# Performance work log

Measured on AMD Instinct MI355X. Metric: run time of the kernel, lower is better.

The kernel has to match this reference:

```python
import jax, jax.numpy as jnp
import numpy as np
import math

B, N, Q, K = 1, 64, 512, 512
C_Q = C_K = C_V = 256
C_HIDDEN = 32
NO_HEADS = 8
HID = C_HIDDEN * NO_HEADS  # 256


def setup_inputs() -> dict:
    key = jax.random.key(0)
    ks = jax.random.split(key, 12)
    inp = {
        "q_x": jax.random.normal(ks[0], (B, N, Q, C_Q), jnp.float32),
        "k_x": jax.random.normal(ks[1], (B, N, K, C_K), jnp.float32),
        "v_x": jax.random.normal(ks[2], (B, N, K, C_V), jnp.float32),
        "bias_mask": jax.random.normal(ks[3], (B, N, 1, 1, K), jnp.float32),
        "bias_pair": jax.random.normal(ks[4], (B, 1, NO_HEADS, Q, K), jnp.float32),
        # projection weights stored [in, out] (torch Linear is [out, in])
        "wq": jax.random.normal(ks[5], (C_Q, HID), jnp.float32) / math.sqrt(C_Q),
        "wk": jax.random.normal(ks[6], (C_K, HID), jnp.float32) / math.sqrt(C_K),
        "wv": jax.random.normal(ks[7], (C_V, HID), jnp.float32) / math.sqrt(C_V),
        # gating: init weights=0, bias=1 in the module; use small random for a non-trivial test
        "wg": jax.random.normal(ks[8], (C_Q, HID), jnp.float32) * 0.02,
        "bg": jnp.ones((HID,), jnp.float32),
        # output: init 'final' (zeros); use small random for a non-trivial test
        "wo": jax.random.normal(ks[9], (HID, C_Q), jnp.float32) * 0.02,
        "bo": jnp.zeros((C_Q,), jnp.float32),
    }
    return inp


def reference(q_x, k_x, v_x, bias_mask, bias_pair, wq, wk, wv, wg, bg, wo, bo):
    h, c = NO_HEADS, C_HIDDEN
    # projections -> [B, N, Q/K, H, C_h]
    q = (q_x @ wq).reshape(*q_x.shape[:-1], h, c) / math.sqrt(c)
    k = (k_x @ wk).reshape(*k_x.shape[:-1], h, c)
    v = (v_x @ wv).reshape(*v_x.shape[:-1], h, c)
    # logits [B, N, H, Q, K] with additive biases
    a = jnp.einsum("bnqhc,bnkhc->bnhqk", q, k) + bias_mask + bias_pair
    a = jax.nn.softmax(a, axis=-1)
    # output [B, N, Q, H, C_h]
    o = jnp.einsum("bnhqk,bnkhc->bnqhc", a, v)
    # gating
    g = jax.nn.sigmoid((q_x @ wg + bg).reshape(*q_x.shape[:-1], h, c))
    o = o * g
    o = o.reshape(*o.shape[:-2], h * c)
    return o @ wo + bo
```

## Files before the change

kernel.cpp:

```cpp
#include <hip/hip_runtime.h>
#include <math.h>

#define NSEQ   64
#define QLEN   512
#define KLEN   512
#define CIN    256
#define HEADS  8
#define CH     32
#define HIDDIM 256
#define M_TOTAL (NSEQ * QLEN)
#define L2E    1.4426950408889634f

typedef _Float16 f16x8 __attribute__((ext_vector_type(8)));
typedef _Float16 f16x4 __attribute__((ext_vector_type(4)));
typedef __fp16   fp16x2 __attribute__((ext_vector_type(2)));
typedef float    f32x4 __attribute__((ext_vector_type(4)));

__device__ __forceinline__ void gload16(const void* g, void* l) {
    __builtin_amdgcn_global_load_lds(
        (const __attribute__((address_space(1))) void*)g,
        (__attribute__((address_space(3))) void*)l, 16, 0, 0);
}

__device__ __forceinline__ float exp2_fast(float x) {
#if __has_builtin(__builtin_amdgcn_exp2f)
    return __builtin_amdgcn_exp2f(x);
#else
    float r; asm("v_exp_f32 %0, %1" : "=v"(r) : "v"(x)); return r;
#endif
}

__global__ __launch_bounds__(256) void wcast_kernel(
    const float* __restrict__ w0, const float* __restrict__ w1,
    const float* __restrict__ w2, const float* __restrict__ w3,
    const float* __restrict__ w4, _Float16* __restrict__ wt)
{
    __shared__ float t[64][65];
    const float* W;
    switch (blockIdx.z) {
        case 0: W = w0; break; case 1: W = w1; break;
        case 2: W = w2; break; case 3: W = w3; break;
        default: W = w4;
    }
    _Float16* WT = wt + (size_t)blockIdx.z * 65536;
    const int i0 = blockIdx.x * 64, o0 = blockIdx.y * 64;
    const int tid = threadIdx.x;
    const int rr = tid >> 4, c4 = tid & 15;
    #pragma unroll
    for (int i = 0; i < 4; ++i) {
        const int row = rr + i * 16;
        *(float4*)&t[row][c4 * 4] = *(const float4*)&W[(size_t)(i0 + row) * 256 + o0 + c4 * 4];
    }
    __syncthreads();
    #pragma unroll
    for (int i = 0; i < 4; ++i) {
        const int row = rr + i * 16;
        f16x4 v;
        #pragma unroll
        for (int j = 0; j < 4; ++j) v[j] = (_Float16)t[c4 * 4 + j][row];
        *(f16x4*)&WT[(size_t)(o0 + row) * 256 + i0 + c4 * 4] = v;
    }
}

__global__ __launch_bounds__(256) void bpfrag_kernel(
    const float* __restrict__ bias_pair, float* __restrict__ frag)
{
    __shared__ float t[64][68];
    const int qb = blockIdx.x, kb = blockIdx.y, h = blockIdx.z;
    const int tid = threadIdx.x;
    #pragma unroll
    for (int i = 0; i < 4; ++i) {
        const int idx = tid + i * 256;
        const int r = idx >> 4, c4 = idx & 15;
        *(float4*)&t[r][c4 * 4] = *(const float4*)
            &bias_pair[((size_t)h * QLEN + qb * 64 + r) * KLEN + kb * 64 + c4 * 4];
    }
    __syncthreads();
    const int lane = tid & 63, w = tid >> 6;
    const int l15 = lane & 15, quad = lane >> 4;
    const int qt = qb * 4 + w;
    #pragma unroll
    for (int kt2 = 0; kt2 < 4; ++kt2) {
        const int kt = kb * 4 + kt2;
        float4 v;
        v.x = (t[w * 16 + l15][kt2 * 16 + quad * 4 + 0] - 4.0f) * L2E;
        v.y = (t[w * 16 + l15][kt2 * 16 + quad * 4 + 1] - 4.0f) * L2E;
        v.z = (t[w * 16 + l15][kt2 * 16 + quad * 4 + 2] - 4.0f) * L2E;
        v.w = (t[w * 16 + l15][kt2 * 16 + quad * 4 + 3] - 4.0f) * L2E;
        *(float4*)&frag[(((size_t)(h * 32 + qt) * 32) + kt) * 256 + lane * 4] = v;
    }
}

__global__ __launch_bounds__(256) void bmscale_kernel(
    const float* __restrict__ bm, float* __restrict__ o)
{
    const int i = blockIdx.x * 256 + threadIdx.x;
    float4 v = *(const float4*)(bm + (size_t)i * 4);
    v.x *= L2E; v.y *= L2E; v.z *= L2E; v.w *= L2E;
    *(float4*)(o + (size_t)i * 4) = v;
}

__global__ __launch_bounds__(256, 3) void proj_gemm_kernel(
    const float* __restrict__ q_x, const float* __restrict__ k_x,
    const float* __restrict__ v_x, const _Float16* __restrict__ wT,
    const float* __restrict__ bg,
    _Float16* __restrict__ oq, _Float16* __restrict__ ok,
    _Float16* __restrict__ ovT, _Float16* __restrict__ og)
{
    __shared__ __attribute__((aligned(16))) _Float16 A_s[2][32 * 256];

    const int combo = blockIdx.x >> 6;
    const int blk   = blockIdx.x & 63;
    const int mode  = combo >> 1;
    const int nhalf = combo & 1;
    const float* A = (mode <= 1) ? q_x : (mode == 2) ? k_x : v_x;
    const _Float16* BT = wT + (size_t)mode * 65536;

    const int tid  = threadIdx.x;
    const int lane = tid & 63, w = tid >> 6;
    const int l15  = lane & 15, quad = lane >> 4;
    const int nw   = nhalf * 128 + w * 32;

    f16x8 bfr[2][8];
    #pragma unroll
    for (int nt = 0; nt < 2; ++nt)
        #pragma unroll
        for (int ks = 0; ks < 8; ++ks)
            bfr[nt][ks] = *(const f16x8*)(BT +
                (size_t)(nw + nt * 16 + l15) * 256 + ks * 32 + quad * 8);

    float bgv[2] = {0.f, 0.f};
    if (mode == 1) { bgv[0] = bg[nw + l15]; bgv[1] = bg[nw + 16 + l15]; }

    const int row_base = blk * 512;

    f32x4 acc[2][2];
    #pragma unroll
    for (int mt = 0; mt < 2; ++mt)
        #pragma unroll
        for (int nt = 0; nt < 2; ++nt) acc[mt][nt] = (f32x4){0.f, 0.f, 0.f, 0.f};

    float4 sreg[8];

    auto gload_panel = [&](int panel) {
        const int row0 = row_base + panel * 32;
        #pragma unroll
        for (int j = 0; j < 4; ++j) {
            const int p = tid + j * 256;
            const int r = p >> 5, c = p & 31;
            const float* ap = A + (size_t)(row0 + r) * 256 + c * 8;
            sreg[j * 2]     = *(const float4*)ap;
            sreg[j * 2 + 1] = *(const float4*)(ap + 4);
        }
    };

    auto swrite_panel = [&](int buf) {
        #pragma unroll
        for (int j = 0; j < 4; ++j) {
            const int p = tid + j * 256;
            const int r = p >> 5, c = p & 31;
            const int cp = c ^ (r & 15);
            f16x8 v;
            v[0] = (_Float16)sreg[j * 2].x;     v[1] = (_Float16)sreg[j * 2].y;
            v[2] = (_Float16)sreg[j * 2].z;     v[3] = (_Float16)sreg[j * 2].w;
            v[4] = (_Float16)sreg[j * 2 + 1].x; v[5] = (_Float16)sreg[j * 2 + 1].y;
            v[6] = (_Float16)sreg[j * 2 + 1].z; v[7] = (_Float16)sreg[j * 2 + 1].w;
            *(f16x8*)&A_s[buf][(r * 32 + cp) * 8] = v;
        }
    };

    gload_panel(0);
    swrite_panel(0);
    __syncthreads();

    for (int i = 0; i < 16; ++i) {
        const int buf = i & 1;
        if (i < 15) gload_panel(i + 1);

        #pragma unroll
        for (int ks = 0; ks < 8; ++ks) {
            f16x8 af[2];
            #pragma unroll
            for (int mt = 0; mt < 2; ++mt) {
                const int r  = mt * 16 + l15;
                const int cp = (ks * 4 + quad) ^ (r & 15);
                af[mt] = *(const f16x8*)&A_s[buf][(r * 32 + cp) * 8];
            }
            #pragma unroll
            for (int mt = 0; mt < 2; ++mt)
                #pragma unroll
                for (int nt = 0; nt < 2; ++nt)
                    acc[mt][nt] = __builtin_amdgcn_mfma_f32_16x16x32_f16(
                        af[mt], bfr[nt][ks], acc[mt][nt], 0, 0, 0);
        }

        const int row0 = row_base + i * 32;
        if (mode == 3) {
            #pragma unroll
            for (int mt = 0; mt < 2; ++mt) {
                #pragma unroll
                for (int nt = 0; nt < 2; ++nt) {
                    const int col  = nw + nt * 16 + l15;
                    const int rowg = row0 + mt * 16 + quad * 4;
                    const int nn = rowg >> 9, kpos = rowg & 511;
                    f16x4 st;
                    #pragma unroll
                    for (int reg = 0; reg < 4; ++reg) st[reg] = (_Float16)acc[mt][nt][reg];
                    *(f16x4*)&ovT[((size_t)(nn * 256 + col)) * 512 + kpos] = st;
                }
            }
        } else {
            _Float16* C = (mode == 0) ? oq : (mode == 1) ? og : ok;
            #pragma unroll
            for (int mt = 0; mt < 2; ++mt) {
                #pragma unroll
                for (int nt = 0; nt < 2; ++nt) {
                    const int col  = nw + nt * 16 + l15;
                    const int rowg = row0 + mt * 16 + quad * 4;
                    #pragma unroll
                    for (int reg = 0; reg < 4; ++reg) {
                        float x = acc[mt][nt][reg];
                        if (mode == 0) x *= 0.2550348614f;
                        if (mode == 1) { x += bgv[nt]; x = 1.0f / (1.0f + __expf(-x)); }
                        C[(size_t)(rowg + reg) * HIDDIM + col] = (_Float16)x;
                    }
                }
            }
        }
        #pragma unroll
        for (int mt = 0; mt < 2; ++mt)
            #pragma unroll
            for (int nt = 0; nt < 2; ++nt) acc[mt][nt] = (f32x4){0.f, 0.f, 0.f, 0.f};

        if (i < 15) swrite_panel(buf ^ 1);
        __syncthreads();
    }
}

__global__ __launch_bounds__(256, 2) void outproj_kernel(
    const _Float16* __restrict__ Ain, const _Float16* __restrict__ BT,
    const float* __restrict__ bias, float* __restrict__ Cout)
{
    __shared__ __attribute__((aligned(16))) _Float16 A_s[2][32 * 256];

    const int blk   = blockIdx.x & 255;
    const int nhalf = blockIdx.x >> 8;
    const int tid  = threadIdx.x;
    const int lane = tid & 63, w = tid >> 6;
    const int l15  = lane & 15, quad = lane >> 4;
    const int nw   = nhalf * 128 + w * 32;

    f16x8 bfr[2][8];
    #pragma unroll
    for (int nt = 0; nt < 2; ++nt)
        #pragma unroll
        for (int ks = 0; ks < 8; ++ks)
            bfr[nt][ks] = *(const f16x8*)(BT +
                (size_t)(nw + nt * 16 + l15) * 256 + ks * 32 + quad * 8);

    const float bv[2] = { bias[nw + l15], bias[nw + 16 + l15] };
    const int row_base = blk * 128;

    f32x4 acc[2][2];
    #pragma unroll
    for (int mt = 0; mt < 2; ++mt)
        #pragma unroll
        for (int nt = 0; nt < 2; ++nt) acc[mt][nt] = (f32x4){0.f, 0.f, 0.f, 0.f};

    auto stage = [&](int panel, int buf) {
        const int row0 = row_base + panel * 32;
        #pragma unroll
        for (int j = 0; j < 4; ++j) {
            const int p = tid + j * 256;
            const int r = p >> 5, c = p & 31;
            const int cl = (c & ~7) | ((c & 7) ^ (r & 7));
            gload16(Ain + (size_t)(row0 + r) * 256 + cl * 8, &A_s[buf][p * 8]);
        }
    };

    stage(0, 0);
    __syncthreads();

    for (int i = 0; i < 4; ++i) {
        if (i < 3) stage(i + 1, (i + 1) & 1);
        const int buf = i & 1;

        #pragma unroll
        for (int ks = 0; ks < 8; ++ks) {
            f16x8 af[2];
            #pragma unroll
            for (int mt = 0; mt < 2; ++mt) {
                const int r = mt * 16 + l15;
                const int c = (ks * 4 + quad) ^ (r & 7);
                af[mt] = *(const f16x8*)&A_s[buf][r * 256 + c * 8];
            }
            #pragma unroll
            for (int mt = 0; mt < 2; ++mt)
                #pragma unroll
                for (int nt = 0; nt < 2; ++nt)
                    acc[mt][nt] = __builtin_amdgcn_mfma_f32_16x16x32_f16(
                        af[mt], bfr[nt][ks], acc[mt][nt], 0, 0, 0);
        }

        const int row0 = row_base + i * 32;
        #pragma unroll
        for (int mt = 0; mt < 2; ++mt) {
            #pragma unroll
            for (int nt = 0; nt < 2; ++nt) {
                const int col  = nw + nt * 16 + l15;
                const int rowg = row0 + mt * 16 + quad * 4;
                #pragma unroll
                for (int reg = 0; reg < 4; ++reg)
                    Cout[(size_t)(rowg + reg) * HIDDIM + col] = acc[mt][nt][reg] + bv[nt];
            }
        }
        #pragma unroll
        for (int mt = 0; mt < 2; ++mt)
            #pragma unroll
            for (int nt = 0; nt < 2; ++nt) acc[mt][nt] = (f32x4){0.f, 0.f, 0.f, 0.f};

        __syncthreads();
    }
}

__global__ __launch_bounds__(256, 4) void attn_kernel(
    const _Float16* __restrict__ qb, const _Float16* __restrict__ kb,
    const _Float16* __restrict__ vT, const _Float16* __restrict__ gb,
    _Float16* __restrict__ ob,
    const float* __restrict__ bm2, const float* __restrict__ bp_frag)
{
    __shared__ _Float16 k_s[128][40];
    __shared__ _Float16 v_s[32][136];

    const int n    = blockIdx.x;
    const int h    = blockIdx.y;
    const int q0   = blockIdx.z * 128;
    const int tid  = threadIdx.x;
    const int lane = tid & 63;
    const int wq   = tid >> 6;
    const int l15  = lane & 15;
    const int quad = lane >> 4;

    f16x8 qf[2];
    #pragma unroll
    for (int qt = 0; qt < 2; ++qt)
        qf[qt] = *(const f16x8*)(qb +
            (size_t)(n * QLEN + q0 + wq * 32 + qt * 16 + l15) * HIDDIM + h * CH + quad * 8);

    const float* bpf = bp_frag +
        ((size_t)(h * 32 + blockIdx.z * 8 + wq * 2) * 32) * 256 + lane * 4;
    const float* bmb = bm2 + n * KLEN + quad * 4;

    f32x4 o_acc[2][2];
    float l_lane[2] = {0.f, 0.f};
    #pragma unroll
    for (int qt = 0; qt < 2; ++qt)
        #pragma unroll
        for (int ct = 0; ct < 2; ++ct) o_acc[qt][ct] = (f32x4){0.f, 0.f, 0.f, 0.f};

    for (int ch = 0; ch < 4; ++ch) {
        __syncthreads();
        #pragma unroll
        for (int i = 0; i < 2; ++i) {
            const int idx = tid + i * 256;
            const int r = idx >> 2, c8 = idx & 3;
            *(uint4*)&k_s[r][c8 * 8] = *(const uint4*)
                (kb + (size_t)(n * KLEN + ch * 128 + r) * HIDDIM + h * CH + c8 * 8);
            const int vr = idx >> 4, vs = idx & 15;
            *(uint4*)&v_s[vr][vs * 8] = *(const uint4*)
                (vT + ((size_t)(n * HEADS + h) * CH + vr) * KLEN + ch * 128 + vs * 8);
        }
        __syncthreads();

        #pragma unroll
        for (int kt = 0; kt < 8; ++kt) {
            const int kti = ch * 8 + kt;
            const f16x8 kf = *(const f16x8*)&k_s[kt * 16 + l15][quad * 8];
            const float4 bm  = *(const float4*)(bmb + ch * 128 + kt * 16);
            const float4 bp0 = *(const float4*)(bpf + (size_t)kti * 256);
            const float4 bp1 = *(const float4*)(bpf + (size_t)(32 + kti) * 256);
            f32x4 c0, c1;
            c0[0] = bm.x + bp0.x; c0[1] = bm.y + bp0.y;
            c0[2] = bm.z + bp0.z; c0[3] = bm.w + bp0.w;
            c1[0] = bm.x + bp1.x; c1[1] = bm.y + bp1.y;
            c1[2] = bm.z + bp1.z; c1[3] = bm.w + bp1.w;
            __builtin_amdgcn_s_setprio(1);
            const f32x4 s0 = __builtin_amdgcn_mfma_f32_16x16x32_f16(kf, qf[0], c0, 0, 0, 0);
            const f32x4 s1 = __builtin_amdgcn_mfma_f32_16x16x32_f16(kf, qf[1], c1, 0, 0, 0);
            __builtin_amdgcn_s_setprio(0);
            const f16x4 bv0 = *(const f16x4*)&v_s[l15][kt * 16 + quad * 4];
            const f16x4 bv1 = *(const f16x4*)&v_s[16 + l15][kt * 16 + quad * 4];
            #pragma unroll
            for (int qt = 0; qt < 2; ++qt) {
                const f32x4 s = qt ? s1 : s0;
                const float p0 = exp2_fast(s[0]);
                const float p1 = exp2_fast(s[1]);
                const float p2 = exp2_fast(s[2]);
                const float p3 = exp2_fast(s[3]);
                l_lane[qt] += (p0 + p1) + (p2 + p3);
                union { f16x4 v; fp16x2 h[2]; } u;
                u.h[0] = __builtin_amdgcn_cvt_pkrtz(p0, p1);
                u.h[1] = __builtin_amdgcn_cvt_pkrtz(p2, p3);
                __builtin_amdgcn_s_setprio(1);
                o_acc[qt][0] = __builtin_amdgcn_mfma_f32_16x16x16f16(u.v, bv0, o_acc[qt][0], 0, 0, 0);
                o_acc[qt][1] = __builtin_amdgcn_mfma_f32_16x16x16f16(u.v, bv1, o_acc[qt][1], 0, 0, 0);
                __builtin_amdgcn_s_setprio(0);
            }
        }
    }

    float invl[2][4];
    #pragma unroll
    for (int qt = 0; qt < 2; ++qt) {
        float lf = l_lane[qt];
        lf += __shfl_xor(lf, 16);
        lf += __shfl_xor(lf, 32);
        #pragma unroll
        for (int reg = 0; reg < 4; ++reg)
            invl[qt][reg] = 1.0f / __shfl(lf, quad * 4 + reg);
    }

    #pragma unroll
    for (int qt = 0; qt < 2; ++qt) {
        #pragma unroll
        for (int ct = 0; ct < 2; ++ct) {
            #pragma unroll
            for (int reg = 0; reg < 4; ++reg) {
                const int row = q0 + wq * 32 + qt * 16 + quad * 4 + reg;
                const size_t idx = (size_t)(n * QLEN + row) * HIDDIM + h * CH + ct * 16 + l15;
                const float g = (float)gb[idx];
                ob[idx] = (_Float16)(o_acc[qt][ct][reg] * invl[qt][reg] * g);
            }
        }
    }
}

extern "C" void kernel_launch(void* const* d_in, const int* in_sizes, int n_in,
                              void* d_out, int out_size, void* d_ws, size_t ws_size,
                              hipStream_t stream)
{
    const float* q_x       = (const float*)d_in[0];
    const float* k_x       = (const float*)d_in[1];
    const float* v_x       = (const float*)d_in[2];
    const float* bias_mask = (const float*)d_in[3];
    const float* bias_pair = (const float*)d_in[4];
    const float* wq        = (const float*)d_in[5];
    const float* wk        = (const float*)d_in[6];
    const float* wv        = (const float*)d_in[7];
    const float* wg        = (const float*)d_in[8];
    const float* bg        = (const float*)d_in[9];
    const float* wo        = (const float*)d_in[10];
    const float* bo        = (const float*)d_in[11];
    float* out = (float*)d_out;

    const size_t BUF = (size_t)M_TOTAL * HIDDIM;
    _Float16* ws_q  = (_Float16*)d_ws;
    _Float16* ws_k  = ws_q + BUF;
    _Float16* ws_vT = ws_k + BUF;
    _Float16* ws_g  = ws_vT + BUF;
    _Float16* ws_o  = ws_g + BUF;
    _Float16* wT    = ws_o + BUF;
    float*    bpf   = (float*)(wT + 5 * 65536);
    float*    bm2   = bpf + (size_t)8 * 512 * 512;

    wcast_kernel<<<dim3(4, 4, 5), 256, 0, stream>>>(wq, wg, wk, wv, wo, wT);
    bpfrag_kernel<<<dim3(8, 8, 8), 256, 0, stream>>>(bias_pair, bpf);
    bmscale_kernel<<<dim3(32), 256, 0, stream>>>(bias_mask, bm2);

    proj_gemm_kernel<<<dim3(512), 256, 0, stream>>>(
        q_x, k_x, v_x, wT, bg, ws_q, ws_k, ws_vT, ws_g);

    attn_kernel<<<dim3(NSEQ, HEADS, QLEN / 128), 256, 0, stream>>>(
        ws_q, ws_k, ws_vT, ws_g, ws_o, bm2, bpf);

    outproj_kernel<<<dim3(512), 256, 0, stream>>>(
        ws_o, wT + 4 * 65536, bo, out);
}
```

Baseline: 257.6 us.

## Swap MFMA operands for row-contiguous vector stores and double GEMM grid sizes

In the projection and output GEMMs, the MFMA operand order is swapped so each lane holds four consecutive columns of one row. The epilogue can then write f16x4 or float4 vector stores instead of scattered scalar stores; the bias is loaded as float4 to match. The grid of both GEMM kernels is doubled, with half the rows per block, to add parallelism, and the output-projection occupancy hint is raised to 3. The trade-off is that the per-block weight-fragment register load is amortized over fewer rows.

```diff
diff --git a/kernel.cpp b/kernel.cpp
--- a/kernel.cpp
+++ b/kernel.cpp
@@ -109,8 +109,8 @@
 {
     __shared__ __attribute__((aligned(16))) _Float16 A_s[2][32 * 256];
 
-    const int combo = blockIdx.x >> 6;
-    const int blk   = blockIdx.x & 63;
+    const int combo = blockIdx.x >> 7;
+    const int blk   = blockIdx.x & 127;
     const int mode  = combo >> 1;
     const int nhalf = combo & 1;
     const float* A = (mode <= 1) ? q_x : (mode == 2) ? k_x : v_x;
@@ -129,10 +129,13 @@
             bfr[nt][ks] = *(const f16x8*)(BT +
                 (size_t)(nw + nt * 16 + l15) * 256 + ks * 32 + quad * 8);
 
-    float bgv[2] = {0.f, 0.f};
-    if (mode == 1) { bgv[0] = bg[nw + l15]; bgv[1] = bg[nw + 16 + l15]; }
-
-    const int row_base = blk * 512;
+    float4 bg4[2] = {{0.f,0.f,0.f,0.f},{0.f,0.f,0.f,0.f}};
+    if (mode == 1) {
+        bg4[0] = *(const float4*)&bg[nw + quad * 4];
+        bg4[1] = *(const float4*)&bg[nw + 16 + quad * 4];
+    }
+
+    const int row_base = blk * 256;
 
     f32x4 acc[2][2];
     #pragma unroll
@@ -173,9 +176,9 @@
     swrite_panel(0);
     __syncthreads();
 
-    for (int i = 0; i < 16; ++i) {
+    for (int i = 0; i < 8; ++i) {
         const int buf = i & 1;
-        if (i < 15) gload_panel(i + 1);
+        if (i < 7) gload_panel(i + 1);
 
         #pragma unroll
         for (int ks = 0; ks < 8; ++ks) {
@@ -186,12 +189,21 @@
                 const int cp = (ks * 4 + quad) ^ (r & 15);
                 af[mt] = *(const f16x8*)&A_s[buf][(r * 32 + cp) * 8];
             }
-            #pragma unroll
-            for (int mt = 0; mt < 2; ++mt)
+            if (mode != 3) {
                 #pragma unroll
-                for (int nt = 0; nt < 2; ++nt)
-                    acc[mt][nt] = __builtin_amdgcn_mfma_f32_16x16x32_f16(
-                        af[mt], bfr[nt][ks], acc[mt][nt], 0, 0, 0);
+                for (int mt = 0; mt < 2; ++mt)
+                    #pragma unroll
+                    for (int nt = 0; nt < 2; ++nt)
+                        acc[mt][nt] = __builtin_amdgcn_mfma_f32_16x16x32_f16(
+                            bfr[nt][ks], af[mt], acc[mt][nt], 0, 0, 0);
+            } else {
+                #pragma unroll
+                for (int mt = 0; mt < 2; ++mt)
+                    #pragma unroll
+                    for (int nt = 0; nt < 2; ++nt)
+                        acc[mt][nt] = __builtin_amdgcn_mfma_f32_16x16x32_f16(
+                            af[mt], bfr[nt][ks], acc[mt][nt], 0, 0, 0);
+            }
         }
 
         const int row0 = row_base + i * 32;
@@ -213,17 +225,22 @@
             _Float16* C = (mode == 0) ? oq : (mode == 1) ? og : ok;
             #pragma unroll
             for (int mt = 0; mt < 2; ++mt) {
+                const int mrow = row0 + mt * 16 + l15;
                 #pragma unroll
                 for (int nt = 0; nt < 2; ++nt) {
-                    const int col  = nw + nt * 16 + l15;
-                    const int rowg = row0 + mt * 16 + quad * 4;
+                    const int colb = nw + nt * 16 + quad * 4;
+                    f16x4 st;
                     #pragma unroll
                     for (int reg = 0; reg < 4; ++reg) {
                         float x = acc[mt][nt][reg];
                         if (mode == 0) x *= 0.2550348614f;
-                        if (mode == 1) { x += bgv[nt]; x = 1.0f / (1.0f + __expf(-x)); }
-                        C[(size_t)(rowg + reg) * HIDDIM + col] = (_Float16)x;
+                        if (mode == 1) {
+                            x += ((const float*)&bg4[nt])[reg];
+                            x = 1.0f / (1.0f + __expf(-x));
+                        }
+                        st[reg] = (_Float16)x;
                     }
+                    *(f16x4*)&C[(size_t)mrow * HIDDIM + colb] = st;
                 }
             }
         }
@@ -232,19 +249,19 @@
             #pragma unroll
             for (int nt = 0; nt < 2; ++nt) acc[mt][nt] = (f32x4){0.f, 0.f, 0.f, 0.f};
 
-        if (i < 15) swrite_panel(buf ^ 1);
+        if (i < 7) swrite_panel(buf ^ 1);
         __syncthreads();
     }
 }
 
-__global__ __launch_bounds__(256, 2) void outproj_kernel(
+__global__ __launch_bounds__(256, 3) void outproj_kernel(
     const _Float16* __restrict__ Ain, const _Float16* __restrict__ BT,
     const float* __restrict__ bias, float* __restrict__ Cout)
 {
     __shared__ __attribute__((aligned(16))) _Float16 A_s[2][32 * 256];
 
-    const int blk   = blockIdx.x & 255;
-    const int nhalf = blockIdx.x >> 8;
+    const int blk   = blockIdx.x & 511;
+    const int nhalf = blockIdx.x >> 9;
     const int tid  = threadIdx.x;
     const int lane = tid & 63, w = tid >> 6;
     const int l15  = lane & 15, quad = lane >> 4;
@@ -258,8 +275,11 @@
             bfr[nt][ks] = *(const f16x8*)(BT +
                 (size_t)(nw + nt * 16 + l15) * 256 + ks * 32 + quad * 8);
 
-    const float bv[2] = { bias[nw + l15], bias[nw + 16 + l15] };
-    const int row_base = blk * 128;
+    const float4 bias4[2] = {
+        *(const float4*)&bias[nw + quad * 4],
+        *(const float4*)&bias[nw + 16 + quad * 4],
+    };
+    const int row_base = blk * 64;
 
     f32x4 acc[2][2];
     #pragma unroll
@@ -281,8 +301,8 @@
     stage(0, 0);
     __syncthreads();
 
-    for (int i = 0; i < 4; ++i) {
-        if (i < 3) stage(i + 1, (i + 1) & 1);
+    for (int i = 0; i < 2; ++i) {
+        if (i < 1) stage(i + 1, (i + 1) & 1);
         const int buf = i & 1;
 
         #pragma unroll
@@ -299,19 +319,22 @@
                 #pragma unroll
                 for (int nt = 0; nt < 2; ++nt)
                     acc[mt][nt] = __builtin_amdgcn_mfma_f32_16x16x32_f16(
-                        af[mt], bfr[nt][ks], acc[mt][nt], 0, 0, 0);
+                        bfr[nt][ks], af[mt], acc[mt][nt], 0, 0, 0);
         }
 
         const int row0 = row_base + i * 32;
         #pragma unroll
         for (int mt = 0; mt < 2; ++mt) {
+            const int mrow = row0 + mt * 16 + l15;
             #pragma unroll
             for (int nt = 0; nt < 2; ++nt) {
-                const int col  = nw + nt * 16 + l15;
-                const int rowg = row0 + mt * 16 + quad * 4;
-                #pragma unroll
-                for (int reg = 0; reg < 4; ++reg)
-                    Cout[(size_t)(rowg + reg) * HIDDIM + col] = acc[mt][nt][reg] + bv[nt];
+                const int colb = nw + nt * 16 + quad * 4;
+                float4 st;
+                st.x = acc[mt][nt][0] + bias4[nt].x;
+                st.y = acc[mt][nt][1] + bias4[nt].y;
+                st.z = acc[mt][nt][2] + bias4[nt].z;
+                st.w = acc[mt][nt][3] + bias4[nt].w;
+                *(float4*)&Cout[(size_t)mrow * HIDDIM + colb] = st;
             }
         }
         #pragma unroll
@@ -467,12 +490,12 @@
     bpfrag_kernel<<<dim3(8, 8, 8), 256, 0, stream>>>(bias_pair, bpf);
     bmscale_kernel<<<dim3(32), 256, 0, stream>>>(bias_mask, bm2);
 
-    proj_gemm_kernel<<<dim3(512), 256, 0, stream>>>(
+    proj_gemm_kernel<<<dim3(1024), 256, 0, stream>>>(
         q_x, k_x, v_x, wT, bg, ws_q, ws_k, ws_vT, ws_g);
 
     attn_kernel<<<dim3(NSEQ, HEADS, QLEN / 128), 256, 0, stream>>>(
         ws_q, ws_k, ws_vT, ws_g, ws_o, bm2, bpf);
 
-    outproj_kernel<<<dim3(512), 256, 0, stream>>>(
+    outproj_kernel<<<dim3(1024), 256, 0, stream>>>(
         ws_o, wT + 4 * 65536, bo, out);
 }
```

New measurement: 257.2 us. Within noise of the previous version (-0.2%).
